# Performance work log

Hardware: AMD Instinct MI355X
Metric: run time of the kernel (lower is better)

The kernel has to match this reference:

```python
import jax, jax.numpy as jnp
import numpy as np

N = 500_000   # nodes
D = 128       # feature dim (init arg d)
B = 1024      # number of graphs / segments
EPS = 1e-6


def setup_inputs() -> dict:
    key = jax.random.key(0)
    k_x, k_b, k_ps, k_qs, k_w, k_bias = jax.random.split(key, 6)
    x = jax.random.normal(k_x, (N, D), dtype=jnp.float32)
    batch = jnp.sort(jax.random.randint(k_b, (N,), 0, B)).astype(jnp.int64)
    ps_raw = jax.random.normal(k_ps, (2,), dtype=jnp.float32)
    qs_raw = jax.random.normal(k_qs, (2,), dtype=jnp.float32)
    W = jax.random.normal(k_w, (D, D), dtype=jnp.float32) / np.sqrt(D)
    b = jax.random.normal(k_bias, (D,), dtype=jnp.float32) * 0.01
    return {"x": x, "batch": batch, "ps_raw": ps_raw, "qs_raw": qs_raw, "W": W, "b": b}


def reference(x, batch, ps_raw, qs_raw, W, b):
    # ps = -Threshold(thr=-50, val=50)(-softplus(ps_raw))
    sp = jax.nn.softplus(ps_raw)
    ps = -jnp.where(-sp > -50.0, -sp, 50.0)
    qs = jnp.tanh(qs_raw)

    # per-graph node counts: global_add_pool(ones)
    nums = jax.ops.segment_sum(jnp.ones(x.shape[0], dtype=x.dtype), batch,
                               num_segments=B)[:, None]            # (B, 1)

    xa = jnp.abs(x) + EPS                                           # (N, D)
    d1 = xa.shape[1] // 2                                           # split feature dim

    # positive branch: exp(p0 * log(x)) == x**p0, summed per graph
    x_pos = jnp.exp(ps[0] * jnp.log(xa[:, :d1]))                    # (N, d1)
    s_pos = jax.ops.segment_sum(x_pos, batch, num_segments=B)       # (B, d1)
    gnp_pos = jnp.exp(jnp.log(s_pos) / ps[0]) / nums ** qs[0]

    # negative branch: plain power / root p-norm form
    s_neg = jax.ops.segment_sum(xa[:, d1:] ** ps[1], batch, num_segments=B)  # (B, D-d1)
    gnp_neg = s_neg ** (1.0 / ps[1]) / nums ** qs[0]

    gnp = jnp.concatenate([gnp_pos, gnp_neg], axis=1)               # (B, D)
    return gnp @ W.T + b
```

## Files before the change

kernel.cpp:

```cpp
#include <hip/hip_runtime.h>
#include <math.h>

#define NSEG   1024
#define DFEAT  128
#define EPS_F  1e-6f
#define NCHUNK 8192

__device__ __forceinline__ float softplus_thr(float v) {
    float sp = log1pf(__expf(v));
    return (sp >= 50.0f) ? -50.0f : sp;
}

__global__ __launch_bounds__(64)
void segsum_kernel(const float* __restrict__ x,
                   const int*   __restrict__ batch,
                   const float* __restrict__ ps_raw,
                   float* __restrict__ s,
                   float* __restrict__ cnt,
                   int n_nodes, int chunk)
{
    const int t = threadIdx.x;
    const int start = blockIdx.x * chunk;
    if (start >= n_nodes) return;
    const int end = min(start + chunk, n_nodes);

    const float p = softplus_thr(ps_raw[(t < 32) ? 0 : 1]);

    const float2* __restrict__ x2 = (const float2*)x;

    int   cur = batch[start];
    float accx = 0.0f, accy = 0.0f;
    int   run = 0;

    for (int n = start; n < end; ++n) {
        const int sg = batch[n];
        if (sg != cur) {
            atomicAdd(&s[(size_t)cur * DFEAT + 2 * t],     accx);
            atomicAdd(&s[(size_t)cur * DFEAT + 2 * t + 1], accy);
            if (t == 0) atomicAdd(&cnt[cur], (float)run);
            accx = 0.0f; accy = 0.0f; run = 0; cur = sg;
        }
        const float2 v = x2[(size_t)n * 64 + t];
        const float ax = fabsf(v.x) + EPS_F;
        const float ay = fabsf(v.y) + EPS_F;
        accx += __expf(p * __logf(ax));
        accy += __expf(p * __logf(ay));
        ++run;
    }
    atomicAdd(&s[(size_t)cur * DFEAT + 2 * t],     accx);
    atomicAdd(&s[(size_t)cur * DFEAT + 2 * t + 1], accy);
    if (t == 0) atomicAdd(&cnt[cur], (float)run);
}

__global__ __launch_bounds__(128)
void finalize_gemm_kernel(const float* __restrict__ s,
                          const float* __restrict__ cnt,
                          const float* __restrict__ ps_raw,
                          const float* __restrict__ qs_raw,
                          const float* __restrict__ W,
                          const float* __restrict__ bias,
                          float* __restrict__ out)
{
    __shared__ float g[DFEAT];
    const int b = blockIdx.x;
    const int i = threadIdx.x;

    const float p  = softplus_thr(ps_raw[(i < 64) ? 0 : 1]);
    const float q0 = tanhf(qs_raw[0]);

    const float n     = cnt[b];
    const float scale = __expf(-q0 * __logf(n));
    const float sv    = s[(size_t)b * DFEAT + i];
    g[i] = __expf(__logf(sv) / p) * scale;
    __syncthreads();

    const float4* __restrict__ W4 = (const float4*)(W + (size_t)i * DFEAT);
    float acc = bias[i];
#pragma unroll
    for (int jj = 0; jj < DFEAT / 4; ++jj) {
        const float4 w = W4[jj];
        acc += g[4 * jj]     * w.x;
        acc += g[4 * jj + 1] * w.y;
        acc += g[4 * jj + 2] * w.z;
        acc += g[4 * jj + 3] * w.w;
    }
    out[(size_t)b * DFEAT + i] = acc;
}

extern "C" void kernel_launch(void* const* d_in, const int* in_sizes, int n_in,
                              void* d_out, int out_size, void* d_ws, size_t ws_size,
                              hipStream_t stream)
{
    const float* x      = (const float*)d_in[0];
    const int*   batch  = (const int*)  d_in[1];
    const float* ps_raw = (const float*)d_in[2];
    const float* qs_raw = (const float*)d_in[3];
    const float* W      = (const float*)d_in[4];
    const float* bias   = (const float*)d_in[5];
    float*       out    = (float*)d_out;

    const int n_nodes = in_sizes[0] / DFEAT;

    float* s   = (float*)d_ws;
    float* cnt = s + (size_t)NSEG * DFEAT;

    hipMemsetAsync(d_ws, 0, sizeof(float) * ((size_t)NSEG * DFEAT + NSEG), stream);

    const int chunk = (n_nodes + NCHUNK - 1) / NCHUNK;
    segsum_kernel<<<NCHUNK, 64, 0, stream>>>(x, batch, ps_raw, s, cnt, n_nodes, chunk);
    finalize_gemm_kernel<<<NSEG, 128, 0, stream>>>(s, cnt, ps_raw, qs_raw, W, bias, out);
}
```

Measured before the change: 371.8 us.

## Replace atomic chunked segment sum with per-segment blocks fused with GEMM

Segment offsets are now found by binary search over the sorted batch array. One 256-thread block per graph then reduces its node rows in four interleaved streams, combines them in shared memory, and applies the power-mean finalize and the W projection in the same kernel. This removes the memset, all global atomics, and the separate finalize launch. In exchange, load balance now depends on segment sizes (1024 blocks, about 490 rows each), and the grid is smaller than the previous 8192 blocks.

```diff
diff --git a/kernel.cpp b/kernel.cpp
--- a/kernel.cpp
+++ b/kernel.cpp
@@ -4,7 +4,6 @@
 #define NSEG   1024
 #define DFEAT  128
 #define EPS_F  1e-6f
-#define NCHUNK 8192
 
 __device__ __forceinline__ float softplus_thr(float v) {
     float sp = log1pf(__expf(v));
@@ -12,79 +11,81 @@
 }
 
 __global__ __launch_bounds__(64)
-void segsum_kernel(const float* __restrict__ x,
-                   const int*   __restrict__ batch,
-                   const float* __restrict__ ps_raw,
-                   float* __restrict__ s,
-                   float* __restrict__ cnt,
-                   int n_nodes, int chunk)
+void seg_offsets_kernel(const int* __restrict__ batch, int n_nodes,
+                        int* __restrict__ off)
 {
+    const int j = blockIdx.x * 64 + threadIdx.x;
+    if (j > NSEG) return;
+    int lo = 0, hi = n_nodes;
+    while (lo < hi) {
+        const int mid = (lo + hi) >> 1;
+        if (batch[mid] < j) lo = mid + 1; else hi = mid;
+    }
+    off[j] = lo;
+}
+
+__global__ __launch_bounds__(256)
+void pool_gemm_kernel(const float* __restrict__ x,
+                      const int*   __restrict__ off,
+                      const float* __restrict__ ps_raw,
+                      const float* __restrict__ qs_raw,
+                      const float* __restrict__ W,
+                      const float* __restrict__ bias,
+                      float* __restrict__ out)
+{
+    const int b = blockIdx.x;
     const int t = threadIdx.x;
-    const int start = blockIdx.x * chunk;
-    if (start >= n_nodes) return;
-    const int end = min(start + chunk, n_nodes);
+    const int l = t & 63;
+    const int r = t >> 6;
 
-    const float p = softplus_thr(ps_raw[(t < 32) ? 0 : 1]);
+    const int start = off[b];
+    const int end   = off[b + 1];
+
+    const float p = softplus_thr(ps_raw[(l < 32) ? 0 : 1]);
 
     const float2* __restrict__ x2 = (const float2*)x;
 
-    int   cur = batch[start];
-    float accx = 0.0f, accy = 0.0f;
-    int   run = 0;
+    float ax = 0.0f, ay = 0.0f;
+#pragma unroll 4
+    for (int n = start + r; n < end; n += 4) {
+        const float2 v = x2[(size_t)n * 64 + l];
+        const float vx = fabsf(v.x) + EPS_F;
+        const float vy = fabsf(v.y) + EPS_F;
+        ax += __expf(p * __logf(vx));
+        ay += __expf(p * __logf(vy));
+    }
 
-    for (int n = start; n < end; ++n) {
-        const int sg = batch[n];
-        if (sg != cur) {
-            atomicAdd(&s[(size_t)cur * DFEAT + 2 * t],     accx);
-            atomicAdd(&s[(size_t)cur * DFEAT + 2 * t + 1], accy);
-            if (t == 0) atomicAdd(&cnt[cur], (float)run);
-            accx = 0.0f; accy = 0.0f; run = 0; cur = sg;
-        }
-        const float2 v = x2[(size_t)n * 64 + t];
-        const float ax = fabsf(v.x) + EPS_F;
-        const float ay = fabsf(v.y) + EPS_F;
-        accx += __expf(p * __logf(ax));
-        accy += __expf(p * __logf(ay));
-        ++run;
-    }
-    atomicAdd(&s[(size_t)cur * DFEAT + 2 * t],     accx);
-    atomicAdd(&s[(size_t)cur * DFEAT + 2 * t + 1], accy);
-    if (t == 0) atomicAdd(&cnt[cur], (float)run);
-}
-
-__global__ __launch_bounds__(128)
-void finalize_gemm_kernel(const float* __restrict__ s,
-                          const float* __restrict__ cnt,
-                          const float* __restrict__ ps_raw,
-                          const float* __restrict__ qs_raw,
-                          const float* __restrict__ W,
-                          const float* __restrict__ bias,
-                          float* __restrict__ out)
-{
-    __shared__ float g[DFEAT];
-    const int b = blockIdx.x;
-    const int i = threadIdx.x;
-
-    const float p  = softplus_thr(ps_raw[(i < 64) ? 0 : 1]);
-    const float q0 = tanhf(qs_raw[0]);
-
-    const float n     = cnt[b];
-    const float scale = __expf(-q0 * __logf(n));
-    const float sv    = s[(size_t)b * DFEAT + i];
-    g[i] = __expf(__logf(sv) / p) * scale;
+    __shared__ float2 part[4][64];
+    __shared__ float  g[DFEAT];
+    part[r][l] = make_float2(ax, ay);
     __syncthreads();
 
-    const float4* __restrict__ W4 = (const float4*)(W + (size_t)i * DFEAT);
-    float acc = bias[i];
+    if (t < 64) {
+        const float2 s0 = part[0][t], s1 = part[1][t];
+        const float2 s2 = part[2][t], s3 = part[3][t];
+        const float sx = (s0.x + s1.x) + (s2.x + s3.x);
+        const float sy = (s0.y + s1.y) + (s2.y + s3.y);
+        const float n     = (float)(end - start);
+        const float q0    = tanhf(qs_raw[0]);
+        const float scale = __expf(-q0 * __logf(n));
+        g[2 * t]     = __expf(__logf(sx) / p) * scale;
+        g[2 * t + 1] = __expf(__logf(sy) / p) * scale;
+    }
+    __syncthreads();
+
+    if (t < DFEAT) {
+        const float4* __restrict__ W4 = (const float4*)(W + (size_t)t * DFEAT);
+        float acc = bias[t];
 #pragma unroll
-    for (int jj = 0; jj < DFEAT / 4; ++jj) {
-        const float4 w = W4[jj];
-        acc += g[4 * jj]     * w.x;
-        acc += g[4 * jj + 1] * w.y;
-        acc += g[4 * jj + 2] * w.z;
-        acc += g[4 * jj + 3] * w.w;
+        for (int jj = 0; jj < DFEAT / 4; ++jj) {
+            const float4 w = W4[jj];
+            acc += g[4 * jj]     * w.x;
+            acc += g[4 * jj + 1] * w.y;
+            acc += g[4 * jj + 2] * w.z;
+            acc += g[4 * jj + 3] * w.w;
+        }
+        out[(size_t)b * DFEAT + t] = acc;
     }
-    out[(size_t)b * DFEAT + i] = acc;
 }
 
 extern "C" void kernel_launch(void* const* d_in, const int* in_sizes, int n_in,
@@ -101,12 +102,8 @@
 
     const int n_nodes = in_sizes[0] / DFEAT;
 
-    float* s   = (float*)d_ws;
-    float* cnt = s + (size_t)NSEG * DFEAT;
+    int* off = (int*)d_ws;
 
-    hipMemsetAsync(d_ws, 0, sizeof(float) * ((size_t)NSEG * DFEAT + NSEG), stream);
-
-    const int chunk = (n_nodes + NCHUNK - 1) / NCHUNK;
-    segsum_kernel<<<NCHUNK, 64, 0, stream>>>(x, batch, ps_raw, s, cnt, n_nodes, chunk);
-    finalize_gemm_kernel<<<NSEG, 128, 0, stream>>>(s, cnt, ps_raw, qs_raw, W, bias, out);
+    seg_offsets_kernel<<<(NSEG + 1 + 63) / 64, 64, 0, stream>>>(batch, n_nodes, off);
+    pool_gemm_kernel<<<NSEG, 256, 0, stream>>>(x, off, ps_raw, qs_raw, W, bias, out);
 }
```

New measurement: 372.9 us. About the same (+0.3%).
